# Optimization experiments

Measured on AMD Instinct MI355X. Metric: run time of the kernel, lower is better.

The kernel has to match this reference:

```python
import jax, jax.numpy as jnp
import numpy as np

N_NODES = 100000
N_EDGES = 1280000
IN_CH = 64
OUT_CH = 64


def setup_inputs() -> dict:
    key = jax.random.key(0)
    k1, k2, k3, k4 = jax.random.split(key, 4)
    x = jax.random.normal(k1, (N_NODES, IN_CH), dtype=jnp.float32)
    edge_index = jax.random.randint(k2, (2, N_EDGES), 0, N_NODES, dtype=jnp.int64)
    # GraphConv params (glorot weight, zero bias)
    scale = jnp.sqrt(6.0 / (IN_CH + OUT_CH)).astype(jnp.float32)
    W = jax.random.uniform(k3, (IN_CH, OUT_CH), dtype=jnp.float32, minval=-scale, maxval=scale)
    b = jnp.zeros((OUT_CH,), dtype=jnp.float32)
    return {"x": x, "edge_index": edge_index, "W": W, "b": b}


def reference(x, edge_index, W, b):
    # DGL GraphConv, norm='both': out = D_in^{-1/2} A^T (D_out^{-1/2} x W) + b
    src, dst = edge_index[0], edge_index[1]
    ones = jnp.ones((src.shape[0],), dtype=x.dtype)
    out_deg = jax.ops.segment_sum(ones, src, num_segments=N_NODES)
    in_deg = jax.ops.segment_sum(ones, dst, num_segments=N_NODES)
    norm_src = jnp.where(out_deg > 0, jax.lax.rsqrt(jnp.maximum(out_deg, 1.0)), 0.0)
    norm_dst = jnp.where(in_deg > 0, jax.lax.rsqrt(jnp.maximum(in_deg, 1.0)), 0.0)
    # in_feats <= out_feats: transform first, then aggregate
    h = (x * norm_src[:, None]) @ W              # [N, OUT_CH]
    msg = h[src]                                 # gather  [E, OUT_CH]
    agg = jax.ops.segment_sum(msg, dst, num_segments=N_NODES)  # scatter-add [N, OUT_CH]
    return agg * norm_dst[:, None] + b
```

## Files before the change

kernel.cpp:

```cpp
#include <hip/hip_runtime.h>
#include <hip/hip_fp16.h>

#define CH 64
#define CAP 32
#define SPILLMAX 4096
#define HBINS 12500
#define HSPAN 25000
#define SLICES 128
#define TILE 2048
#define EPT 8
#define BSH 9
#define BKT 512

__global__ __launch_bounds__(256) void histA_kernel(const int* __restrict__ src,
                                                    const int* __restrict__ dst,
                                                    int* __restrict__ partial,
                                                    int* __restrict__ tileHist,
                                                    int* __restrict__ nspill,
                                                    int E, int N, int R, int NT)
{
    __shared__ int h[HBINS];
    int tid = threadIdx.x;
    int bid = blockIdx.x;
    if (bid < NT) {
        if (bid == 0 && tid == 0) nspill[0] = 0;
        h[tid] = 0;
        __syncthreads();
        int e0 = bid * TILE + tid * EPT;
        if (e0 + EPT <= E) {
            const int4* dp = (const int4*)(dst + e0);
            int4 a = dp[0], b = dp[1];
            atomicAdd(&h[a.x >> BSH], 1); atomicAdd(&h[a.y >> BSH], 1);
            atomicAdd(&h[a.z >> BSH], 1); atomicAdd(&h[a.w >> BSH], 1);
            atomicAdd(&h[b.x >> BSH], 1); atomicAdd(&h[b.y >> BSH], 1);
            atomicAdd(&h[b.z >> BSH], 1); atomicAdd(&h[b.w >> BSH], 1);
        } else {
            for (int k = e0; k < E && k < e0 + EPT; ++k) atomicAdd(&h[dst[k] >> BSH], 1);
        }
        __syncthreads();
        tileHist[bid * 256 + tid] = h[tid];
    } else {
        int hb = bid - NT;
        int r  = hb % R;
        int sl = hb / R;
        int lo = r * HSPAN;
        int hi = min(lo + HSPAN, N);
        for (int i = tid; i < HBINS; i += 256) h[i] = 0;
        __syncthreads();
        int per = (E + SLICES - 1) / SLICES;
        int sb = sl * per, se = min(sb + per, E);
        for (int e = sb + tid * 4; e < se; e += 256 * 4) {
            if (e + 4 <= se) {
                int4 v = *(const int4*)(src + e);
                if (v.x >= lo && v.x < hi) { int i0 = v.x - lo; atomicAdd(&h[i0 >> 1], 1u << ((i0 & 1) << 4)); }
                if (v.y >= lo && v.y < hi) { int i1 = v.y - lo; atomicAdd(&h[i1 >> 1], 1u << ((i1 & 1) << 4)); }
                if (v.z >= lo && v.z < hi) { int i2 = v.z - lo; atomicAdd(&h[i2 >> 1], 1u << ((i2 & 1) << 4)); }
                if (v.w >= lo && v.w < hi) { int i3 = v.w - lo; atomicAdd(&h[i3 >> 1], 1u << ((i3 & 1) << 4)); }
            } else {
                for (int k = e; k < se; ++k) {
                    int sv = src[k];
                    if (sv >= lo && sv < hi) { int ii = sv - lo; atomicAdd(&h[ii >> 1], 1u << ((ii & 1) << 4)); }
                }
            }
        }
        __syncthreads();
        int* pp = partial + (size_t)hb * HBINS;
        for (int i = tid; i < HBINS; i += 256) pp[i] = h[i];
    }
}

__global__ __launch_bounds__(256) void rpscaleB_kernel(const int* __restrict__ partial,
                                                       const float* __restrict__ x,
                                                       __half* __restrict__ xh,
                                                       int* __restrict__ tileHist,
                                                       int* __restrict__ totals,
                                                       int N, int R, int NT, int NPB)
{
    __shared__ float nsl[256];
    __shared__ int sm[256];
    int tid = threadIdx.x;
    int bid = blockIdx.x;
    if (bid < NPB) {
        int n0 = bid * 256;
        int n = n0 + tid;
        if (n < N) {
            int r = n / HSPAN;
            int idx = n - r * HSPAN;
            int word = idx >> 1;
            int sh = (idx & 1) << 4;
            int s = 0;
            #pragma unroll 8
            for (int sl = 0; sl < SLICES; ++sl)
                s += (partial[(size_t)(sl * R + r) * HBINS + word] >> sh) & 0xFFFF;
            nsl[tid] = (s > 0) ? rsqrtf((float)s) : 0.0f;
        } else {
            nsl[tid] = 0.0f;
        }
        __syncthreads();
        int sub = tid & 7;
        int nl0 = tid >> 3;
        for (int p = 0; p < 8; ++p) {
            int nl = p * 32 + nl0;
            int node = n0 + nl;
            if (node >= N) break;
            float ns = nsl[nl];
            const float4* xp = (const float4*)(x + (size_t)node * CH + sub * 8);
            float4 a = xp[0], b = xp[1];
            __half2 h0 = __floats2half2_rn(a.x * ns, a.y * ns);
            __half2 h1 = __floats2half2_rn(a.z * ns, a.w * ns);
            __half2 h2 = __floats2half2_rn(b.x * ns, b.y * ns);
            __half2 h3 = __floats2half2_rn(b.z * ns, b.w * ns);
            uint4 u;
            u.x = (unsigned)__half_as_ushort(h0.x) | ((unsigned)__half_as_ushort(h0.y) << 16);
            u.y = (unsigned)__half_as_ushort(h1.x) | ((unsigned)__half_as_ushort(h1.y) << 16);
            u.z = (unsigned)__half_as_ushort(h2.x) | ((unsigned)__half_as_ushort(h2.y) << 16);
            u.w = (unsigned)__half_as_ushort(h3.x) | ((unsigned)__half_as_ushort(h3.y) << 16);
            *(uint4*)(xh + (size_t)node * CH + sub * 8) = u;
        }
    } else {
        int b = bid - NPB;
        int C = (NT + 255) / 256;
        int vals[8];
        int s = 0;
        for (int k = 0; k < C; ++k) {
            int t = tid * C + k;
            vals[k] = (t < NT) ? tileHist[t * 256 + b] : 0;
            s += vals[k];
        }
        sm[tid] = s;
        __syncthreads();
        for (int d = 1; d < 256; d <<= 1) {
            int v = (tid >= d) ? sm[tid - d] : 0;
            __syncthreads();
            sm[tid] += v;
            __syncthreads();
        }
        int off = (tid > 0) ? sm[tid - 1] : 0;
        for (int k = 0; k < C; ++k) {
            int t = tid * C + k;
            if (t < NT) { tileHist[t * 256 + b] = off; off += vals[k]; }
        }
        if (tid == 255) totals[b] = sm[255];
    }
}

__global__ __launch_bounds__(256) void binC_kernel(const int* __restrict__ src,
                                                   const int* __restrict__ dst,
                                                   const int* __restrict__ tileBase,
                                                   const int* __restrict__ totals,
                                                   int* __restrict__ sorted, int E, int NB)
{
    __shared__ int sm[256];
    __shared__ int gb[256];
    __shared__ int lcnt[256];
    __shared__ int lbase[256];
    __shared__ int slotVal[TILE];
    int tid = threadIdx.x;
    int t = blockIdx.x;
    sm[tid] = (tid < NB) ? totals[tid] : 0;
    lcnt[tid] = 0;
    __syncthreads();
    for (int d = 1; d < 256; d <<= 1) {
        int v = (tid >= d) ? sm[tid - d] : 0;
        __syncthreads();
        sm[tid] += v;
        __syncthreads();
    }
    int bb = (tid > 0) ? sm[tid - 1] : 0;
    gb[tid] = (tid < NB) ? bb + tileBase[t * 256 + tid] : 0;
    __syncthreads();
    int e0 = t * TILE + tid * EPT;
    int s[EPT], d[EPT], rk[EPT], pb[EPT];
    int nk = 0;
    if (e0 + EPT <= E) {
        const int4* sp = (const int4*)(src + e0);
        const int4* dp = (const int4*)(dst + e0);
        int4 a = sp[0], b = sp[1], c = dp[0], f = dp[1];
        s[0]=a.x; s[1]=a.y; s[2]=a.z; s[3]=a.w; s[4]=b.x; s[5]=b.y; s[6]=b.z; s[7]=b.w;
        d[0]=c.x; d[1]=c.y; d[2]=c.z; d[3]=c.w; d[4]=f.x; d[5]=f.y; d[6]=f.z; d[7]=f.w;
        nk = EPT;
    } else {
        for (int k = 0; e0 + k < E && k < EPT; ++k) { s[k] = src[e0+k]; d[k] = dst[e0+k]; nk++; }
    }
    for (int k = 0; k < nk; ++k) {
        pb[k] = d[k] >> BSH;
        rk[k] = atomicAdd(&lcnt[pb[k]], 1);
    }
    __syncthreads();
    sm[tid] = lcnt[tid];
    __syncthreads();
    for (int dd = 1; dd < 256; dd <<= 1) {
        int v = (tid >= dd) ? sm[tid - dd] : 0;
        __syncthreads();
        sm[tid] += v;
        __syncthreads();
    }
    lbase[tid] = (tid > 0) ? sm[tid - 1] : 0;
    int total = sm[255];
    __syncthreads();
    for (int k = 0; k < nk; ++k)
        slotVal[lbase[pb[k]] + rk[k]] = (s[k] << BSH) | (d[k] & (BKT - 1));
    __syncthreads();
    for (int i = tid; i < total; i += 256) {
        int lo = 0, hi = 255;
        #pragma unroll
        for (int st = 0; st < 8; ++st) {
            int mid = (lo + hi + 1) >> 1;
            if (lbase[mid] <= i) lo = mid; else hi = mid - 1;
        }
        sorted[gb[lo] + (i - lbase[lo])] = slotVal[i];
    }
}

__global__ __launch_bounds__(256) void binD_kernel(const int* __restrict__ sorted,
                                                   const int* __restrict__ totals,
                                                   int* __restrict__ bucket,
                                                   int* __restrict__ cnt,
                                                   int* __restrict__ spill,
                                                   int* __restrict__ nspill, int N, int NB)
{
    __shared__ int sm[256];
    __shared__ int lc[BKT];
    int b = blockIdx.x, tid = threadIdx.x;
    sm[tid] = (tid < NB) ? totals[tid] : 0;
    lc[tid] = 0; lc[tid + 256] = 0;
    __syncthreads();
    for (int d = 1; d < 256; d <<= 1) {
        int v = (tid >= d) ? sm[tid - d] : 0;
        __syncthreads();
        sm[tid] += v;
        __syncthreads();
    }
    int beg = (b > 0) ? sm[b - 1] : 0;
    int end = sm[b];
    int nbase = b << BSH;
    for (int i = beg + tid; i < end; i += 256) {
        int v = sorted[i];
        int sv = v >> BSH;
        int dl = v & (BKT - 1);
        int pos = atomicAdd(&lc[dl], 1);
        if (pos < CAP) {
            bucket[(size_t)(nbase + dl) * CAP + pos] = sv;
        } else {
            int sp = atomicAdd(nspill, 1);
            if (sp < SPILLMAX) { spill[2*sp] = nbase + dl; spill[2*sp+1] = sv; }
        }
    }
    __syncthreads();
    int n0 = nbase + tid;
    if (n0 < N) cnt[n0] = lc[tid];
    int n1 = nbase + 256 + tid;
    if (n1 < N) cnt[n1] = lc[256 + tid];
}

__global__ __launch_bounds__(256) void agg_kernel(const __half* __restrict__ xh,
                                                  const int* __restrict__ bucket,
                                                  const int* __restrict__ cnt,
                                                  const int* __restrict__ spill,
                                                  const int* __restrict__ nspill,
                                                  __half* __restrict__ aggh, int N)
{
    int node = (blockIdx.x * blockDim.x + threadIdx.x) >> 5;
    int sl = threadIdx.x & 31;
    if (node >= N) return;
    int c = cnt[node];
    int m = (c < CAP) ? c : CAP;
    const int* bp = bucket + (size_t)node * CAP;
    float ax0 = 0, ay0 = 0, ax1 = 0, ay1 = 0, ax2 = 0, ay2 = 0, ax3 = 0, ay3 = 0;
    int j = 0;
    for (; j + 8 <= m; j += 8) {
        int4 va = *(const int4*)(bp + j);
        int4 vb = *(const int4*)(bp + j + 4);
        float2 f0 = __half22float2(*(const __half2*)(xh + (size_t)va.x * CH + sl * 2));
        float2 f1 = __half22float2(*(const __half2*)(xh + (size_t)va.y * CH + sl * 2));
        float2 f2 = __half22float2(*(const __half2*)(xh + (size_t)va.z * CH + sl * 2));
        float2 f3 = __half22float2(*(const __half2*)(xh + (size_t)va.w * CH + sl * 2));
        float2 f4 = __half22float2(*(const __half2*)(xh + (size_t)vb.x * CH + sl * 2));
        float2 f5 = __half22float2(*(const __half2*)(xh + (size_t)vb.y * CH + sl * 2));
        float2 f6 = __half22float2(*(const __half2*)(xh + (size_t)vb.z * CH + sl * 2));
        float2 f7 = __half22float2(*(const __half2*)(xh + (size_t)vb.w * CH + sl * 2));
        ax0 += f0.x + f4.x; ay0 += f0.y + f4.y;
        ax1 += f1.x + f5.x; ay1 += f1.y + f5.y;
        ax2 += f2.x + f6.x; ay2 += f2.y + f6.y;
        ax3 += f3.x + f7.x; ay3 += f3.y + f7.y;
    }
    for (; j + 4 <= m; j += 4) {
        int4 va = *(const int4*)(bp + j);
        float2 f0 = __half22float2(*(const __half2*)(xh + (size_t)va.x * CH + sl * 2));
        float2 f1 = __half22float2(*(const __half2*)(xh + (size_t)va.y * CH + sl * 2));
        float2 f2 = __half22float2(*(const __half2*)(xh + (size_t)va.z * CH + sl * 2));
        float2 f3 = __half22float2(*(const __half2*)(xh + (size_t)va.w * CH + sl * 2));
        ax0 += f0.x; ay0 += f0.y;
        ax1 += f1.x; ay1 += f1.y;
        ax2 += f2.x; ay2 += f2.y;
        ax3 += f3.x; ay3 += f3.y;
    }
    for (; j < m; ++j) {
        float2 f = __half22float2(*(const __half2*)(xh + (size_t)bp[j] * CH + sl * 2));
        ax0 += f.x; ay0 += f.y;
    }
    if (c > CAP) {
        int ns = *nspill;
        if (ns > SPILLMAX) ns = SPILLMAX;
        for (int i = 0; i < ns; ++i) {
            if (spill[2 * i] == node) {
                float2 f = __half22float2(*(const __half2*)(xh + (size_t)spill[2 * i + 1] * CH + sl * 2));
                ax0 += f.x; ay0 += f.y;
            }
        }
    }
    float nd = (c > 0) ? rsqrtf((float)c) : 0.0f;
    float rx = ((ax0 + ax1) + (ax2 + ax3)) * nd;
    float ry = ((ay0 + ay1) + (ay2 + ay3)) * nd;
    *(__half2*)(aggh + (size_t)node * CH + sl * 2) = __floats2half2_rn(rx, ry);
}

__global__ __launch_bounds__(256) void gemm_out_kernel(const __half* __restrict__ aggh,
                                                       const float* __restrict__ W,
                                                       const float* __restrict__ bias,
                                                       float* __restrict__ out, int N)
{
    int g = blockIdx.x * 256 + threadIdx.x;
    int waveId = __builtin_amdgcn_readfirstlane(g >> 6);
    int lane = threadIdx.x & 63;
    int quarter = waveId & 3;
    int row = ((waveId >> 2) << 6) + lane;
    if (row >= N) return;
    const int cbase = quarter * 16;
    float acc[16];
    #pragma unroll
    for (int i = 0; i < 16; ++i) acc[i] = 0.0f;
    const __half* xp = aggh + (size_t)row * CH;
    for (int k0 = 0; k0 < CH; k0 += 8) {
        uint4 u = *(const uint4*)(xp + k0);
        const __half2* hp = (const __half2*)&u;
        float xk[8];
        #pragma unroll
        for (int j = 0; j < 4; ++j) {
            float2 f = __half22float2(hp[j]);
            xk[2 * j] = f.x; xk[2 * j + 1] = f.y;
        }
        #pragma unroll
        for (int kk = 0; kk < 8; ++kk) {
            const float* wrow = W + (k0 + kk) * CH + cbase;
            #pragma unroll
            for (int q = 0; q < 4; ++q) {
                float4 w = *(const float4*)(wrow + q * 4);
                acc[q * 4 + 0] += xk[kk] * w.x;
                acc[q * 4 + 1] += xk[kk] * w.y;
                acc[q * 4 + 2] += xk[kk] * w.z;
                acc[q * 4 + 3] += xk[kk] * w.w;
            }
        }
    }
    float* op = out + (size_t)row * CH + cbase;
    #pragma unroll
    for (int q = 0; q < 4; ++q) {
        float4 b = *(const float4*)(bias + cbase + q * 4);
        float4 o;
        o.x = acc[q * 4 + 0] + b.x;
        o.y = acc[q * 4 + 1] + b.y;
        o.z = acc[q * 4 + 2] + b.z;
        o.w = acc[q * 4 + 3] + b.w;
        *(float4*)(op + q * 4) = o;
    }
}

extern "C" void kernel_launch(void* const* d_in, const int* in_sizes, int n_in,
                              void* d_out, int out_size, void* d_ws, size_t ws_size,
                              hipStream_t stream)
{
    const float* x    = (const float*)d_in[0];
    const int*   edge = (const int*)d_in[1];
    const float* W    = (const float*)d_in[2];
    const float* bias = (const float*)d_in[3];
    float* out = (float*)d_out;

    int N = in_sizes[0] / CH;
    int E = in_sizes[1] / 2;
    const int* src = edge;
    const int* dst = edge + E;
    int R   = (N + HSPAN - 1) / HSPAN;
    int NT  = (E + TILE - 1) / TILE;
    int NB  = (N + BKT - 1) >> BSH;
    int NPB = (N + 255) / 256;

    int* nspill  = (int*)d_ws;
    int* spill   = nspill + 64;
    int* cnt     = spill + 2 * SPILLMAX;
    int* bucket  = cnt + N;
    int* partial = bucket + (size_t)N * CAP;
    int* tileHist = partial + (size_t)R * SLICES * HBINS;
    int* totals   = tileHist + NT * 256;
    int* sorted   = partial;
    size_t endoff = (char*)(totals + 320) - (char*)d_ws;
    size_t xoff = (endoff + 255) & ~(size_t)255;
    __half* xh = (__half*)((char*)d_ws + xoff);
    size_t aoff = ((xoff + (size_t)N * CH * sizeof(__half)) + 255) & ~(size_t)255;
    __half* aggh = (__half*)((char*)d_ws + aoff);

    histA_kernel<<<NT + R * SLICES, 256, 0, stream>>>(src, dst, partial, tileHist,
                                                      nspill, E, N, R, NT);
    rpscaleB_kernel<<<NPB + NB, 256, 0, stream>>>(partial, x, xh, tileHist, totals,
                                                  N, R, NT, NPB);
    binC_kernel<<<NT, 256, 0, stream>>>(src, dst, tileHist, totals, sorted, E, NB);
    binD_kernel<<<NB, 256, 0, stream>>>(sorted, totals, bucket, cnt, spill, nspill, N, NB);
    agg_kernel<<<((size_t)N * 32 + 255) / 256, 256, 0, stream>>>(xh, bucket, cnt, spill,
                                                                 nspill, aggh, N);
    int nwaves = 4 * ((N + 63) / 64);
    gemm_out_kernel<<<(nwaves + 3) / 4, 256, 0, stream>>>(aggh, W, bias, out, N);
}
```

Measured before the change: 107.8 us.

## Fuse neighbor aggregation with output GEMM via shared memory; halve histogram slices

Merges the gather-aggregate kernel and the dense output GEMM into one kernel. Each block aggregates 8 nodes into a shared-memory tile, then multiplies that tile by W directly. This drops the fp16 aggregate round trip through global memory and one kernel launch, and keeps the aggregate in fp32 before the GEMM. It also halves SLICES in the histogram stage, which shrinks the partial buffers but gives fewer blocks there. The risk is that the GEMM phase rereads W from global or cache for every block and does less work per thread.

Result: slower. 167.4 us (+55.3%).

```diff
diff --git a/kernel.cpp b/kernel.cpp
--- a/kernel.cpp
+++ b/kernel.cpp
@@ -6,7 +6,7 @@
 #define SPILLMAX 4096
 #define HBINS 12500
 #define HSPAN 25000
-#define SLICES 128
+#define SLICES 64
 #define TILE 2048
 #define EPT 8
 #define BSH 9
@@ -253,117 +253,91 @@
     if (n1 < N) cnt[n1] = lc[256 + tid];
 }
 
-__global__ __launch_bounds__(256) void agg_kernel(const __half* __restrict__ xh,
-                                                  const int* __restrict__ bucket,
-                                                  const int* __restrict__ cnt,
-                                                  const int* __restrict__ spill,
-                                                  const int* __restrict__ nspill,
-                                                  __half* __restrict__ aggh, int N)
-{
-    int node = (blockIdx.x * blockDim.x + threadIdx.x) >> 5;
-    int sl = threadIdx.x & 31;
-    if (node >= N) return;
-    int c = cnt[node];
-    int m = (c < CAP) ? c : CAP;
-    const int* bp = bucket + (size_t)node * CAP;
-    float ax0 = 0, ay0 = 0, ax1 = 0, ay1 = 0, ax2 = 0, ay2 = 0, ax3 = 0, ay3 = 0;
-    int j = 0;
-    for (; j + 8 <= m; j += 8) {
-        int4 va = *(const int4*)(bp + j);
-        int4 vb = *(const int4*)(bp + j + 4);
-        float2 f0 = __half22float2(*(const __half2*)(xh + (size_t)va.x * CH + sl * 2));
-        float2 f1 = __half22float2(*(const __half2*)(xh + (size_t)va.y * CH + sl * 2));
-        float2 f2 = __half22float2(*(const __half2*)(xh + (size_t)va.z * CH + sl * 2));
-        float2 f3 = __half22float2(*(const __half2*)(xh + (size_t)va.w * CH + sl * 2));
-        float2 f4 = __half22float2(*(const __half2*)(xh + (size_t)vb.x * CH + sl * 2));
-        float2 f5 = __half22float2(*(const __half2*)(xh + (size_t)vb.y * CH + sl * 2));
-        float2 f6 = __half22float2(*(const __half2*)(xh + (size_t)vb.z * CH + sl * 2));
-        float2 f7 = __half22float2(*(const __half2*)(xh + (size_t)vb.w * CH + sl * 2));
-        ax0 += f0.x + f4.x; ay0 += f0.y + f4.y;
-        ax1 += f1.x + f5.x; ay1 += f1.y + f5.y;
-        ax2 += f2.x + f6.x; ay2 += f2.y + f6.y;
-        ax3 += f3.x + f7.x; ay3 += f3.y + f7.y;
-    }
-    for (; j + 4 <= m; j += 4) {
-        int4 va = *(const int4*)(bp + j);
-        float2 f0 = __half22float2(*(const __half2*)(xh + (size_t)va.x * CH + sl * 2));
-        float2 f1 = __half22float2(*(const __half2*)(xh + (size_t)va.y * CH + sl * 2));
-        float2 f2 = __half22float2(*(const __half2*)(xh + (size_t)va.z * CH + sl * 2));
-        float2 f3 = __half22float2(*(const __half2*)(xh + (size_t)va.w * CH + sl * 2));
-        ax0 += f0.x; ay0 += f0.y;
-        ax1 += f1.x; ay1 += f1.y;
-        ax2 += f2.x; ay2 += f2.y;
-        ax3 += f3.x; ay3 += f3.y;
-    }
-    for (; j < m; ++j) {
-        float2 f = __half22float2(*(const __half2*)(xh + (size_t)bp[j] * CH + sl * 2));
-        ax0 += f.x; ay0 += f.y;
-    }
-    if (c > CAP) {
-        int ns = *nspill;
-        if (ns > SPILLMAX) ns = SPILLMAX;
-        for (int i = 0; i < ns; ++i) {
-            if (spill[2 * i] == node) {
-                float2 f = __half22float2(*(const __half2*)(xh + (size_t)spill[2 * i + 1] * CH + sl * 2));
-                ax0 += f.x; ay0 += f.y;
+__global__ __launch_bounds__(256) void aggemm_kernel(const __half* __restrict__ xh,
+                                                     const int* __restrict__ bucket,
+                                                     const int* __restrict__ cnt,
+                                                     const int* __restrict__ spill,
+                                                     const int* __restrict__ nspill,
+                                                     const float* __restrict__ W,
+                                                     const float* __restrict__ bias,
+                                                     float* __restrict__ out, int N)
+{
+    __shared__ float accum[8][CH];
+    int tid = threadIdx.x;
+    int hw = tid >> 5;
+    int sl = tid & 31;
+    int node = blockIdx.x * 8 + hw;
+    if (node < N) {
+        int c = cnt[node];
+        int m = (c < CAP) ? c : CAP;
+        const int* bp = bucket + (size_t)node * CAP;
+        float ax0 = 0, ay0 = 0, ax1 = 0, ay1 = 0, ax2 = 0, ay2 = 0, ax3 = 0, ay3 = 0;
+        int j = 0;
+        for (; j + 8 <= m; j += 8) {
+            int4 va = *(const int4*)(bp + j);
+            int4 vb = *(const int4*)(bp + j + 4);
+            float2 f0 = __half22float2(*(const __half2*)(xh + (size_t)va.x * CH + sl * 2));
+            float2 f1 = __half22float2(*(const __half2*)(xh + (size_t)va.y * CH + sl * 2));
+            float2 f2 = __half22float2(*(const __half2*)(xh + (size_t)va.z * CH + sl * 2));
+            float2 f3 = __half22float2(*(const __half2*)(xh + (size_t)va.w * CH + sl * 2));
+            float2 f4 = __half22float2(*(const __half2*)(xh + (size_t)vb.x * CH + sl * 2));
+            float2 f5 = __half22float2(*(const __half2*)(xh + (size_t)vb.y * CH + sl * 2));
+            float2 f6 = __half22float2(*(const __half2*)(xh + (size_t)vb.z * CH + sl * 2));
+            float2 f7 = __half22float2(*(const __half2*)(xh + (size_t)vb.w * CH + sl * 2));
+            ax0 += f0.x + f4.x; ay0 += f0.y + f4.y;
+            ax1 += f1.x + f5.x; ay1 += f1.y + f5.y;
+            ax2 += f2.x + f6.x; ay2 += f2.y + f6.y;
+            ax3 += f3.x + f7.x; ay3 += f3.y + f7.y;
+        }
+        for (; j + 4 <= m; j += 4) {
+            int4 va = *(const int4*)(bp + j);
+            float2 f0 = __half22float2(*(const __half2*)(xh + (size_t)va.x * CH + sl * 2));
+            float2 f1 = __half22float2(*(const __half2*)(xh + (size_t)va.y * CH + sl * 2));
+            float2 f2 = __half22float2(*(const __half2*)(xh + (size_t)va.z * CH + sl * 2));
+            float2 f3 = __half22float2(*(const __half2*)(xh + (size_t)va.w * CH + sl * 2));
+            ax0 += f0.x; ay0 += f0.y;
+            ax1 += f1.x; ay1 += f1.y;
+            ax2 += f2.x; ay2 += f2.y;
+            ax3 += f3.x; ay3 += f3.y;
+        }
+        for (; j < m; ++j) {
+            float2 f = __half22float2(*(const __half2*)(xh + (size_t)bp[j] * CH + sl * 2));
+            ax0 += f.x; ay0 += f.y;
+        }
+        if (c > CAP) {
+            int ns = *nspill;
+            if (ns > SPILLMAX) ns = SPILLMAX;
+            for (int i = 0; i < ns; ++i) {
+                if (spill[2 * i] == node) {
+                    float2 f = __half22float2(*(const __half2*)(xh + (size_t)spill[2 * i + 1] * CH + sl * 2));
+                    ax0 += f.x; ay0 += f.y;
+                }
             }
         }
-    }
-    float nd = (c > 0) ? rsqrtf((float)c) : 0.0f;
-    float rx = ((ax0 + ax1) + (ax2 + ax3)) * nd;
-    float ry = ((ay0 + ay1) + (ay2 + ay3)) * nd;
-    *(__half2*)(aggh + (size_t)node * CH + sl * 2) = __floats2half2_rn(rx, ry);
-}
-
-__global__ __launch_bounds__(256) void gemm_out_kernel(const __half* __restrict__ aggh,
-                                                       const float* __restrict__ W,
-                                                       const float* __restrict__ bias,
-                                                       float* __restrict__ out, int N)
-{
-    int g = blockIdx.x * 256 + threadIdx.x;
-    int waveId = __builtin_amdgcn_readfirstlane(g >> 6);
-    int lane = threadIdx.x & 63;
-    int quarter = waveId & 3;
-    int row = ((waveId >> 2) << 6) + lane;
-    if (row >= N) return;
-    const int cbase = quarter * 16;
-    float acc[16];
-    #pragma unroll
-    for (int i = 0; i < 16; ++i) acc[i] = 0.0f;
-    const __half* xp = aggh + (size_t)row * CH;
-    for (int k0 = 0; k0 < CH; k0 += 8) {
-        uint4 u = *(const uint4*)(xp + k0);
-        const __half2* hp = (const __half2*)&u;
-        float xk[8];
-        #pragma unroll
-        for (int j = 0; j < 4; ++j) {
-            float2 f = __half22float2(hp[j]);
-            xk[2 * j] = f.x; xk[2 * j + 1] = f.y;
-        }
-        #pragma unroll
-        for (int kk = 0; kk < 8; ++kk) {
-            const float* wrow = W + (k0 + kk) * CH + cbase;
-            #pragma unroll
-            for (int q = 0; q < 4; ++q) {
-                float4 w = *(const float4*)(wrow + q * 4);
-                acc[q * 4 + 0] += xk[kk] * w.x;
-                acc[q * 4 + 1] += xk[kk] * w.y;
-                acc[q * 4 + 2] += xk[kk] * w.z;
-                acc[q * 4 + 3] += xk[kk] * w.w;
-            }
-        }
-    }
-    float* op = out + (size_t)row * CH + cbase;
-    #pragma unroll
-    for (int q = 0; q < 4; ++q) {
-        float4 b = *(const float4*)(bias + cbase + q * 4);
-        float4 o;
-        o.x = acc[q * 4 + 0] + b.x;
-        o.y = acc[q * 4 + 1] + b.y;
-        o.z = acc[q * 4 + 2] + b.z;
-        o.w = acc[q * 4 + 3] + b.w;
-        *(float4*)(op + q * 4) = o;
-    }
+        float nd = (c > 0) ? rsqrtf((float)c) : 0.0f;
+        float2 rr;
+        rr.x = ((ax0 + ax1) + (ax2 + ax3)) * nd;
+        rr.y = ((ay0 + ay1) + (ay2 + ay3)) * nd;
+        *(float2*)&accum[hw][sl * 2] = rr;
+    }
+    __syncthreads();
+    int r = tid >> 5;
+    int cp = (tid & 31) * 2;
+    int onode = blockIdx.x * 8 + r;
+    if (onode >= N) return;
+    float a0 = 0.0f, a1 = 0.0f;
+    #pragma unroll 8
+    for (int k = 0; k < CH; ++k) {
+        float a = accum[r][k];
+        float2 w = *(const float2*)(W + k * CH + cp);
+        a0 += a * w.x;
+        a1 += a * w.y;
+    }
+    float2 b = *(const float2*)(bias + cp);
+    float2 o;
+    o.x = a0 + b.x;
+    o.y = a1 + b.y;
+    *(float2*)(out + (size_t)onode * CH + cp) = o;
 }
 
 extern "C" void kernel_launch(void* const* d_in, const int* in_sizes, int n_in,
@@ -396,8 +370,6 @@
     size_t endoff = (char*)(totals + 320) - (char*)d_ws;
     size_t xoff = (endoff + 255) & ~(size_t)255;
     __half* xh = (__half*)((char*)d_ws + xoff);
-    size_t aoff = ((xoff + (size_t)N * CH * sizeof(__half)) + 255) & ~(size_t)255;
-    __half* aggh = (__half*)((char*)d_ws + aoff);
 
     histA_kernel<<<NT + R * SLICES, 256, 0, stream>>>(src, dst, partial, tileHist,
                                                       nspill, E, N, R, NT);
@@ -405,8 +377,6 @@
                                                   N, R, NT, NPB);
     binC_kernel<<<NT, 256, 0, stream>>>(src, dst, tileHist, totals, sorted, E, NB);
     binD_kernel<<<NB, 256, 0, stream>>>(sorted, totals, bucket, cnt, spill, nspill, N, NB);
-    agg_kernel<<<((size_t)N * 32 + 255) / 256, 256, 0, stream>>>(xh, bucket, cnt, spill,
-                                                                 nspill, aggh, N);
-    int nwaves = 4 * ((N + 63) / 64);
-    gemm_out_kernel<<<(nwaves + 3) / 4, 256, 0, stream>>>(aggh, W, bias, out, N);
-}
+    aggemm_kernel<<<(N + 7) / 8, 256, 0, stream>>>(xh, bucket, cnt, spill, nspill,
+                                                   W, bias, out, N);
+}
```

## Stage per-node buckets in LDS, sort sources, write buckets with vector stores

Applied to the files above, without the earlier changes.

binD now processes the 512-node bucket range in two halves of 256 nodes. Each half collects source indices into a padded shared-memory buffer, insertion-sorts each node's list, and writes the full CAP-wide bucket row with int4 stores instead of scattered 4-byte global writes. Sorted sources should give the aggregation gathers better locality. The cost is reading the sorted input twice, per-thread serial sorting, and more LDS use, which lowers occupancy. SLICES is also halved, which changes work partitioning in an earlier stage.

Result: slower. 166.6 us (+54.6%).

```diff
diff --git a/kernel.cpp b/kernel.cpp
--- a/kernel.cpp
+++ b/kernel.cpp
@@ -6,7 +6,7 @@
 #define SPILLMAX 4096
 #define HBINS 12500
 #define HSPAN 25000
-#define SLICES 128
+#define SLICES 64
 #define TILE 2048
 #define EPT 8
 #define BSH 9
@@ -220,10 +220,10 @@
                                                    int* __restrict__ nspill, int N, int NB)
 {
     __shared__ int sm[256];
-    __shared__ int lc[BKT];
+    __shared__ int lc[256];
+    __shared__ int lbuf[256 * (CAP + 1)];
     int b = blockIdx.x, tid = threadIdx.x;
     sm[tid] = (tid < NB) ? totals[tid] : 0;
-    lc[tid] = 0; lc[tid + 256] = 0;
     __syncthreads();
     for (int d = 1; d < 256; d <<= 1) {
         int v = (tid >= d) ? sm[tid - d] : 0;
@@ -234,23 +234,46 @@
     int beg = (b > 0) ? sm[b - 1] : 0;
     int end = sm[b];
     int nbase = b << BSH;
-    for (int i = beg + tid; i < end; i += 256) {
-        int v = sorted[i];
-        int sv = v >> BSH;
-        int dl = v & (BKT - 1);
-        int pos = atomicAdd(&lc[dl], 1);
-        if (pos < CAP) {
-            bucket[(size_t)(nbase + dl) * CAP + pos] = sv;
-        } else {
-            int sp = atomicAdd(nspill, 1);
-            if (sp < SPILLMAX) { spill[2*sp] = nbase + dl; spill[2*sp+1] = sv; }
-        }
-    }
-    __syncthreads();
-    int n0 = nbase + tid;
-    if (n0 < N) cnt[n0] = lc[tid];
-    int n1 = nbase + 256 + tid;
-    if (n1 < N) cnt[n1] = lc[256 + tid];
+    for (int half = 0; half < 2; ++half) {
+        lc[tid] = 0;
+        __syncthreads();
+        for (int i = beg + tid; i < end; i += 256) {
+            int v = sorted[i];
+            int dl = v & (BKT - 1);
+            if ((dl >> 8) == half) {
+                int dh = dl & 255;
+                int sv = v >> BSH;
+                int pos = atomicAdd(&lc[dh], 1);
+                if (pos < CAP) {
+                    lbuf[dh * (CAP + 1) + pos] = sv;
+                } else {
+                    int sp = atomicAdd(nspill, 1);
+                    if (sp < SPILLMAX) { spill[2*sp] = nbase + dl; spill[2*sp+1] = sv; }
+                }
+            }
+        }
+        __syncthreads();
+        int mm = lc[tid]; if (mm > CAP) mm = CAP;
+        int* L = &lbuf[tid * (CAP + 1)];
+        for (int i = 1; i < mm; ++i) {
+            int key = L[i];
+            int j = i - 1;
+            while (j >= 0 && L[j] > key) { L[j + 1] = L[j]; --j; }
+            L[j + 1] = key;
+        }
+        int nodeg = nbase + half * 256 + tid;
+        if (nodeg < N) {
+            cnt[nodeg] = lc[tid];
+            int* gB = bucket + (size_t)nodeg * CAP;
+            #pragma unroll
+            for (int k = 0; k < CAP; k += 4) {
+                int4 w;
+                w.x = L[k]; w.y = L[k + 1]; w.z = L[k + 2]; w.w = L[k + 3];
+                *(int4*)(gB + k) = w;
+            }
+        }
+        __syncthreads();
+    }
 }
 
 __global__ __launch_bounds__(256) void agg_kernel(const __half* __restrict__ xh,
```
